# Optimization experiments

Hardware: AMD Instinct MI355X
Metric: run time of the kernel (lower is better)

Reference implementation:

```python
import jax, jax.numpy as jnp
import numpy as np

ANCHOR_NUM = 8
CLASS_NUM = 2
IN_DIM = 1024

def setup_inputs() -> dict:
    key = jax.random.key(0)
    k1, k2, k3, k4 = jax.random.split(key, 4)
    batch_input = jax.random.normal(k1, (64, 512, IN_DIM), dtype=jnp.float32)
    # labels in {-1, 0, 1}: -1 = padding, 0 = negative anchor, 1 = positive anchor
    anchor_labels = jax.random.randint(k2, (64, 512, ANCHOR_NUM), 0, 3, dtype=jnp.int64 if jax.config.read('jax_enable_x64') else jnp.int32) - 1
    lim = 1.0 / np.sqrt(IN_DIM)
    W = jax.random.uniform(k3, (IN_DIM, ANCHOR_NUM * CLASS_NUM), dtype=jnp.float32, minval=-lim, maxval=lim)
    b = jax.random.uniform(k4, (ANCHOR_NUM * CLASS_NUM,), dtype=jnp.float32, minval=-lim, maxval=lim)
    return {"batch_input": batch_input, "W": W, "b": b, "anchor_labels": anchor_labels}

def reference(batch_input, W, b, anchor_labels):
    B, S, _ = batch_input.shape
    # logits: (B, S, anchor_num, class_num)
    logits = (jnp.einsum('bsd,dk->bsk', batch_input, W) + b).reshape(B, S, ANCHOR_NUM, CLASS_NUM)
    predict_label = jnp.argmax(logits, axis=3)  # (B, S, A)
    valid = (anchor_labels != -1)
    labels = jnp.maximum(anchor_labels, 0)  # safe class index for padded entries
    logp = jax.nn.log_softmax(logits, axis=-1)
    nll = -jnp.take_along_axis(logp, labels[..., None].astype(jnp.int32), axis=-1)[..., 0]
    # CrossEntropyLoss (mean) over all non-padding anchors == eval-path gather + CE
    vf = valid.astype(logits.dtype)
    loss = jnp.sum(nll * vf) / jnp.maximum(jnp.sum(vf), 1.0)
    # candidate mask stands in for candidate_idx (positive predictions, non-padding)
    candidate_mask = (predict_label == 1) & valid
    return loss, predict_label, candidate_mask
```

## Files before the change

kernel.cpp:

```cpp
#include <hip/hip_runtime.h>
#include <math.h>


#define ROWS   64
#define NW     8
#define KSLICE 128
#define CHUNK  32
#define NCH    (KSLICE/CHUNK)
#define XSTR   36
#define RSTR   136

__global__ __launch_bounds__(512, 4)
void rpn_main(const float* __restrict__ x, const float* __restrict__ W,
              const float* __restrict__ b, const int* __restrict__ lab,
              float* __restrict__ out, float* __restrict__ ws)
{
    __shared__ float xs[NW * ROWS * XSTR];
    float* red = xs;

    const int tid  = threadIdx.x;
    const int lane = tid & 63;
    const int ks   = __builtin_amdgcn_readfirstlane(tid >> 6);
    const int row0 = blockIdx.x * ROWS;

    float* slab = xs + ks * (ROWS * XSTR);
    const float* gbase = x + (size_t)row0 * 1024 + ks * KSLICE;

    float acc[16];
#pragma unroll
    for (int c = 0; c < 16; ++c) acc[c] = 0.f;

    float4 pf[8];
#pragma unroll
    for (int j = 0; j < 8; ++j) {
        int fl = j * 64 + lane;
        pf[j] = *(const float4*)(gbase + (size_t)(fl >> 3) * 1024 + (fl & 7) * 4);
    }

#pragma unroll 1
    for (int ch = 0; ch < NCH; ++ch) {
#pragma unroll
        for (int j = 0; j < 8; ++j) {
            int fl = j * 64 + lane;
            *(float4*)(slab + (fl >> 3) * XSTR + (fl & 7) * 4) = pf[j];
        }
        if (ch + 1 < NCH) {
            const float* g = gbase + (ch + 1) * CHUNK;
#pragma unroll
            for (int j = 0; j < 8; ++j) {
                int fl = j * 64 + lane;
                pf[j] = *(const float4*)(g + (size_t)(fl >> 3) * 1024 + (fl & 7) * 4);
            }
        }
        const float* xrow = slab + lane * XSTR;
        const float* wk   = W + (size_t)(ks * KSLICE + ch * CHUNK) * 16;
#pragma unroll
        for (int t4 = 0; t4 < 8; ++t4) {
            float4 xq = *(const float4*)(xrow + t4 * 4);
#pragma unroll
            for (int i = 0; i < 4; ++i) {
                float xv = (&xq.x)[i];
                const float* wr = wk + (t4 * 4 + i) * 16;
#pragma unroll
                for (int c = 0; c < 16; ++c)
                    acc[c] = fmaf(xv, wr[c], acc[c]);
            }
        }
    }

    __syncthreads();
    {
        float* rp = red + lane * RSTR + ks * 16;
        *(float4*)(rp + 0)  = make_float4(acc[0],  acc[1],  acc[2],  acc[3]);
        *(float4*)(rp + 4)  = make_float4(acc[4],  acc[5],  acc[6],  acc[7]);
        *(float4*)(rp + 8)  = make_float4(acc[8],  acc[9],  acc[10], acc[11]);
        *(float4*)(rp + 12) = make_float4(acc[12], acc[13], acc[14], acc[15]);
    }
    __syncthreads();

    if (tid < ROWS) {
        const int row = row0 + tid;
        float L[16];
#pragma unroll
        for (int c = 0; c < 16; ++c) {
            float s = 0.f;
#pragma unroll
            for (int k = 0; k < NW; ++k) s += red[tid * RSTR + k * 16 + c];
            L[c] = s + b[c];
        }

        const int* labp  = lab + (size_t)row * 8;
        float*     predp = out + 1 + (size_t)row * 8;
        float*     maskp = out + 1 + 262144 + (size_t)row * 8;

        float lsum = 0.f, lcnt = 0.f;
#pragma unroll
        for (int a = 0; a < 8; ++a) {
            float l0 = L[2 * a], l1 = L[2 * a + 1];
            int   lb = labp[a];
            int   pred  = (l1 > l0) ? 1 : 0;
            int   valid = (lb != -1);
            float m   = fmaxf(l0, l1);
            float lse = m + logf(expf(l0 - m) + expf(l1 - m));
            float nll = lse - ((lb == 1) ? l1 : l0);
            if (valid) { lsum += nll; lcnt += 1.f; }
            predp[a] = (float)pred;
            maskp[a] = (pred && valid) ? 1.f : 0.f;
        }

#pragma unroll
        for (int off = 32; off > 0; off >>= 1) {
            lsum += __shfl_down(lsum, off, 64);
            lcnt += __shfl_down(lcnt, off, 64);
        }
        if (tid == 0) {
            atomicAdd(&ws[0], lsum);
            atomicAdd(&ws[1], lcnt);
        }
    }
}

__global__ void rpn_final(const float* __restrict__ ws, float* __restrict__ out)
{
    out[0] = ws[0] / fmaxf(ws[1], 1.f);
}

extern "C" void kernel_launch(void* const* d_in, const int* in_sizes, int n_in,
                              void* d_out, int out_size, void* d_ws, size_t ws_size,
                              hipStream_t stream)
{
    const float* x   = (const float*)d_in[0];
    const float* W   = (const float*)d_in[1];
    const float* b   = (const float*)d_in[2];
    const int*   lab = (const int*)d_in[3];
    float* out = (float*)d_out;
    float* ws  = (float*)d_ws;

    hipMemsetAsync(ws, 0, 2 * sizeof(float), stream);
    rpn_main<<<dim3(512), dim3(512), 0, stream>>>(x, W, b, lab, out, ws);
    rpn_final<<<dim3(1), dim3(1), 0, stream>>>(ws, out);
}
```

Baseline: 237.9 us.

## Load x rows directly into registers instead of staging through LDS

```diff
diff --git a/kernel.cpp b/kernel.cpp
--- a/kernel.cpp
+++ b/kernel.cpp
@@ -5,68 +5,67 @@
 #define ROWS   64
 #define NW     8
 #define KSLICE 128
-#define CHUNK  32
-#define NCH    (KSLICE/CHUNK)
-#define XSTR   36
+#define KCH    16
+#define NCH    (KSLICE/KCH)
 #define RSTR   136
 
-__global__ __launch_bounds__(512, 4)
+__global__ __launch_bounds__(512, 2)
 void rpn_main(const float* __restrict__ x, const float* __restrict__ W,
               const float* __restrict__ b, const int* __restrict__ lab,
               float* __restrict__ out, float* __restrict__ ws)
 {
-    __shared__ float xs[NW * ROWS * XSTR];
-    float* red = xs;
+    __shared__ float red[ROWS * RSTR];
 
     const int tid  = threadIdx.x;
     const int lane = tid & 63;
     const int ks   = __builtin_amdgcn_readfirstlane(tid >> 6);
     const int row0 = blockIdx.x * ROWS;
 
-    float* slab = xs + ks * (ROWS * XSTR);
-    const float* gbase = x + (size_t)row0 * 1024 + ks * KSLICE;
+    const float* xp = x + (size_t)(row0 + lane) * 1024 + ks * KSLICE;
+    const float* wk = W + (size_t)(ks * KSLICE) * 16;
 
     float acc[16];
 #pragma unroll
     for (int c = 0; c < 16; ++c) acc[c] = 0.f;
 
-    float4 pf[8];
+    float4 pf[4];
 #pragma unroll
-    for (int j = 0; j < 8; ++j) {
-        int fl = j * 64 + lane;
-        pf[j] = *(const float4*)(gbase + (size_t)(fl >> 3) * 1024 + (fl & 7) * 4);
-    }
+    for (int j = 0; j < 4; ++j) pf[j] = *(const float4*)(xp + j * 4);
+
+#define FMA16(V, WROW)                                            \
+    do {                                                          \
+        const float* _w = (WROW);                                 \
+        _Pragma("unroll")                                         \
+        for (int c = 0; c < 16; ++c)                              \
+            acc[c] = fmaf((V), _w[c], acc[c]);                    \
+    } while (0)
 
 #pragma unroll 1
-    for (int ch = 0; ch < NCH; ++ch) {
+    for (int ch = 0; ch < NCH - 1; ++ch) {
+        const float* wc = wk + ch * KCH * 16;
+        const float* gn = xp + (ch + 1) * KCH;
 #pragma unroll
-        for (int j = 0; j < 8; ++j) {
-            int fl = j * 64 + lane;
-            *(float4*)(slab + (fl >> 3) * XSTR + (fl & 7) * 4) = pf[j];
-        }
-        if (ch + 1 < NCH) {
-            const float* g = gbase + (ch + 1) * CHUNK;
-#pragma unroll
-            for (int j = 0; j < 8; ++j) {
-                int fl = j * 64 + lane;
-                pf[j] = *(const float4*)(g + (size_t)(fl >> 3) * 1024 + (fl & 7) * 4);
-            }
-        }
-        const float* xrow = slab + lane * XSTR;
-        const float* wk   = W + (size_t)(ks * KSLICE + ch * CHUNK) * 16;
-#pragma unroll
-        for (int t4 = 0; t4 < 8; ++t4) {
-            float4 xq = *(const float4*)(xrow + t4 * 4);
-#pragma unroll
-            for (int i = 0; i < 4; ++i) {
-                float xv = (&xq.x)[i];
-                const float* wr = wk + (t4 * 4 + i) * 16;
-#pragma unroll
-                for (int c = 0; c < 16; ++c)
-                    acc[c] = fmaf(xv, wr[c], acc[c]);
-            }
+        for (int j = 0; j < 4; ++j) {
+            float4 v = pf[j];
+            pf[j] = *(const float4*)(gn + j * 4);
+            FMA16(v.x, wc + (j * 4 + 0) * 16);
+            FMA16(v.y, wc + (j * 4 + 1) * 16);
+            FMA16(v.z, wc + (j * 4 + 2) * 16);
+            FMA16(v.w, wc + (j * 4 + 3) * 16);
         }
     }
+    {
+        const float* wc = wk + (NCH - 1) * KCH * 16;
+#pragma unroll
+        for (int j = 0; j < 4; ++j) {
+            float4 v = pf[j];
+            FMA16(v.x, wc + (j * 4 + 0) * 16);
+            FMA16(v.y, wc + (j * 4 + 1) * 16);
+            FMA16(v.z, wc + (j * 4 + 2) * 16);
+            FMA16(v.w, wc + (j * 4 + 3) * 16);
+        }
+    }
+#undef FMA16
 
     __syncthreads();
     {
```

Measured after the change: 211.8 us. -11.0%, faster.
